# Kernel optimization log

Hardware: AMD Instinct MI355X
Metric: run time of the kernel (lower is better)

## Reference

```python
import jax, jax.numpy as jnp
import numpy as np

B, D, E, K, H, C = 8192, 1024, 8, 2, 2048, 512
LN_EPS = 1e-5


def setup_inputs() -> dict:
    key = jax.random.key(0)
    ks = jax.random.split(key, 6)
    s = 0.02
    return {
        "x": jax.random.normal(ks[0], (B, D), dtype=jnp.float32),
        "Wr": jax.random.normal(ks[1], (E, D), dtype=jnp.float32) * s,  # router weight [E,D]
        "br": jnp.zeros((E,), dtype=jnp.float32),
        "gamma": jnp.ones((E, D), dtype=jnp.float32),   # per-expert LayerNorm scale
        "beta": jnp.zeros((E, D), dtype=jnp.float32),   # per-expert LayerNorm shift
        "W1": jax.random.normal(ks[2], (E, H, D), dtype=jnp.float32) * s,
        "b1": jnp.zeros((E, H), dtype=jnp.float32),
        "W2": jax.random.normal(ks[3], (E, C, H), dtype=jnp.float32) * s,
        "b2": jnp.zeros((E, C), dtype=jnp.float32),
    }


def reference(x, Wr, br, gamma, beta, W1, b1, W2, b2):
    # Router + top-k gating (softmax over the k selected logits only)
    router_logits = x @ Wr.T + br                       # [B,E]
    topk_vals, topk_idx = jax.lax.top_k(router_logits, K)  # [B,K]
    topk_w = jax.nn.softmax(topk_vals, axis=-1)         # [B,K]
    # Dense gate [B,E]: gate[b,e] = sum_j topk_w[b,j] * (topk_idx[b,j]==e)
    gate = (jax.nn.one_hot(topk_idx, E, dtype=x.dtype) * topk_w[..., None]).sum(axis=1)

    # LayerNorm statistics are expert-independent; affine is per-expert
    mu = x.mean(axis=-1, keepdims=True)
    var = ((x - mu) ** 2).mean(axis=-1, keepdims=True)
    xn = (x - mu) * jax.lax.rsqrt(var + LN_EPS)          # [B,D]

    out = jnp.zeros((x.shape[0], C), dtype=x.dtype)
    for e in range(E):  # small fixed expert count
        xe = xn * gamma[e] + beta[e]                     # [B,D]
        h = jax.nn.gelu(xe @ W1[e].T + b1[e], approximate=False)  # [B,H]
        y = h @ W2[e].T + b2[e]                          # [B,C]
        out = out + gate[:, e:e + 1] * y
    return out
```

## Files before the change

kernel.cpp:

```cpp
#include <hip/hip_runtime.h>
#include <hip/hip_bf16.h>
#include <math.h>

#define B_TOK 8192
#define DDIM 1024
#define NEXP 8
#define HDIM 2048
#define CDIM 512
#define LN_EPS 1e-5f
#define MAXT256 72
#define MAXROWS (MAXT256 * 256)

typedef __attribute__((ext_vector_type(4))) float f32x4;
typedef __attribute__((ext_vector_type(8))) short bf16x8;

__device__ __forceinline__ unsigned short f2bf(float f) {
  __hip_bfloat16 h = __float2bfloat16(f);
  return *reinterpret_cast<unsigned short*>(&h);
}
__device__ __forceinline__ float bf2f(unsigned short u) {
  unsigned int x = ((unsigned int)u) << 16;
  return *reinterpret_cast<float*>(&x);
}

__device__ __forceinline__ float gelu_f(float v) {
  const float t = __builtin_fmaf(0.044715f * v, v, 1.0f);
  const float u = -1.5957691216f * v * t;
  return v * __builtin_amdgcn_rcpf(1.0f + __expf(u));
}

__device__ __forceinline__ void gload_lds16(const unsigned short* g, unsigned short* l) {
  __builtin_amdgcn_global_load_lds(
      (const __attribute__((address_space(1))) unsigned int*)g,
      (__attribute__((address_space(3))) unsigned int*)l, 16, 0, 0);
}

__global__ __launch_bounds__(256) void router_ln_kernel(
    const float* __restrict__ x, const float* __restrict__ Wr,
    const float* __restrict__ br, int* __restrict__ eidx,
    float* __restrict__ wgt, unsigned short* __restrict__ xn) {
  const int wid = threadIdx.x >> 6;
  const int lane = threadIdx.x & 63;
  const int tok = blockIdx.x * 4 + wid;

  const float4* xr = reinterpret_cast<const float4*>(x + (size_t)tok * DDIM);
  float4 xv[4];
  float sum = 0.f, sumsq = 0.f;
  float dot[NEXP];
#pragma unroll
  for (int e = 0; e < NEXP; ++e) dot[e] = 0.f;

#pragma unroll
  for (int i = 0; i < 4; ++i) {
    const int f = i * 64 + lane;
    float4 v = xr[f];
    xv[i] = v;
    sum += v.x + v.y + v.z + v.w;
    sumsq += v.x * v.x + v.y * v.y + v.z * v.z + v.w * v.w;
#pragma unroll
    for (int e = 0; e < NEXP; ++e) {
      float4 w = reinterpret_cast<const float4*>(Wr + e * DDIM)[f];
      dot[e] += v.x * w.x + v.y * w.y + v.z * w.z + v.w * w.w;
    }
  }
#pragma unroll
  for (int off = 32; off > 0; off >>= 1) {
    sum += __shfl_xor(sum, off);
    sumsq += __shfl_xor(sumsq, off);
#pragma unroll
    for (int e = 0; e < NEXP; ++e) dot[e] += __shfl_xor(dot[e], off);
  }
  const float mu = sum * (1.f / DDIM);
  const float var = sumsq * (1.f / DDIM) - mu * mu;
  const float rs = rsqrtf(var + LN_EPS);

  float lg[NEXP];
#pragma unroll
  for (int e = 0; e < NEXP; ++e) lg[e] = dot[e] + br[e];

  int i1 = 0; float v1 = lg[0];
#pragma unroll
  for (int e = 1; e < NEXP; ++e) { if (lg[e] > v1) { v1 = lg[e]; i1 = e; } }
  int i2 = -1; float v2 = -3.4e38f;
#pragma unroll
  for (int e = 0; e < NEXP; ++e) { if (e != i1 && lg[e] > v2) { v2 = lg[e]; i2 = e; } }

  const float e2 = __expf(v2 - v1);
  const float inv = 1.f / (1.f + e2);
  if (lane == 0) {
    eidx[tok * 2] = i1; eidx[tok * 2 + 1] = i2;
    wgt[tok * 2] = inv; wgt[tok * 2 + 1] = e2 * inv;
  }

  unsigned short* xnr = xn + (size_t)tok * DDIM;
#pragma unroll
  for (int i = 0; i < 4; ++i) {
    const int f = i * 64 + lane;
    float4 v = xv[i];
    ushort4 o;
    o.x = f2bf((v.x - mu) * rs);
    o.y = f2bf((v.y - mu) * rs);
    o.z = f2bf((v.z - mu) * rs);
    o.w = f2bf((v.w - mu) * rs);
    reinterpret_cast<ushort4*>(xnr)[f] = o;
  }
}

__global__ __launch_bounds__(256) void sort_kernel(
    const int* __restrict__ eidx,
    int* __restrict__ tokRow,
    int* __restrict__ slot2row,
    int* __restrict__ tileExp,
    int* __restrict__ nTilesOut) {
  __shared__ int cnt[NEXP], segBase[NEXP], cur[NEXP];
  const int tid = threadIdx.x;
  if (tid < NEXP) { cnt[tid] = 0; cur[tid] = 0; }
  __syncthreads();
  for (int t = tid; t < B_TOK * 2; t += 256)
    atomicAdd(&cnt[eidx[t]], 1);
  __syncthreads();
  if (tid == 0) {
    int c = 0;
    for (int e = 0; e < NEXP; ++e) {
      segBase[e] = c;
      const int nt = (cnt[e] + 255) >> 8;
      for (int t = 0; t < nt; ++t) tileExp[(c >> 8) + t] = e;
      for (int p = c + cnt[e]; p < c + nt * 256; ++p) tokRow[p] = 0;
      c += nt * 256;
    }
    *nTilesOut = c >> 8;
  }
  __syncthreads();
  for (int t = tid; t < B_TOK * 2; t += 256) {
    const int e = eidx[t];
    const int pos = segBase[e] + atomicAdd(&cur[e], 1);
    tokRow[pos] = t >> 1;
    slot2row[t] = pos;
  }
}

__global__ __launch_bounds__(256) void prep_w1_kernel(
    const float* __restrict__ W1, const float* __restrict__ gamma,
    const float* __restrict__ beta, const float* __restrict__ b1,
    unsigned short* __restrict__ W1g, float* __restrict__ c1) {
  const int eh = blockIdx.x;
  const int e = eh >> 11;
  const int tid = threadIdx.x;

  float4 w = reinterpret_cast<const float4*>(W1 + (size_t)eh * DDIM)[tid];
  float4 g = reinterpret_cast<const float4*>(gamma + (size_t)e * DDIM)[tid];
  float4 bt = reinterpret_cast<const float4*>(beta + (size_t)e * DDIM)[tid];

  ushort4 o;
  o.x = f2bf(w.x * g.x); o.y = f2bf(w.y * g.y);
  o.z = f2bf(w.z * g.z); o.w = f2bf(w.w * g.w);
  reinterpret_cast<ushort4*>(W1g + (size_t)eh * DDIM)[tid] = o;

  float p = w.x * bt.x + w.y * bt.y + w.z * bt.z + w.w * bt.w;
#pragma unroll
  for (int off = 32; off > 0; off >>= 1) p += __shfl_xor(p, off);
  __shared__ float red[4];
  const int lane = tid & 63, wv = tid >> 6;
  if (lane == 0) red[wv] = p;
  __syncthreads();
  if (tid == 0) c1[eh] = b1[eh] + red[0] + red[1] + red[2] + red[3];
}

__global__ __launch_bounds__(256) void prep_w2_kernel(
    const float* __restrict__ W2, unsigned short* __restrict__ W2b) {
  const int idx = blockIdx.x * 256 + threadIdx.x;
  float4 w = reinterpret_cast<const float4*>(W2)[idx];
  ushort4 o;
  o.x = f2bf(w.x); o.y = f2bf(w.y); o.z = f2bf(w.z); o.w = f2bf(w.w);
  reinterpret_cast<ushort4*>(W2b)[idx] = o;
}

#define BM 128
#define BN 128
#define BKK 64

__global__ __launch_bounds__(256) void gemm1_gelu_kernel(
    const unsigned short* __restrict__ A,
    const unsigned short* __restrict__ W1g,
    const float* __restrict__ c1,
    const int* __restrict__ tokRow, const int* __restrict__ tileExp,
    const int* __restrict__ nTiles,
    unsigned short* __restrict__ Hout) {
  const int flat = blockIdx.x;
  const int by = flat & 15;
  const int bx = flat >> 4;
  if ((bx >> 1) >= *nTiles) return;
  const int e = tileExp[bx >> 1];

  __shared__ unsigned short lA[BM * BKK];
  __shared__ unsigned short lB[BN * BKK];
  const int tid = threadIdx.x;
  const int lane = tid & 63;
  const int wid = tid >> 6;
  const int wr = wid >> 1, wc = wid & 1;
  const int l15 = lane & 15, l4 = lane >> 4;

  const unsigned short* Bbase = W1g + ((size_t)e * HDIM + (size_t)by * BN) * DDIM;

  const int r = tid >> 3;
  const int swz = ((tid & 7) ^ (r & 7)) * 8;
  const int dst = (tid & 7) * 8;
  int aRow[4];
#pragma unroll
  for (int i = 0; i < 4; ++i) aRow[i] = tokRow[bx * BM + i * 32 + r];

  f32x4 acc[4][4];
#pragma unroll
  for (int n = 0; n < 4; ++n)
#pragma unroll
    for (int m = 0; m < 4; ++m)
#pragma unroll
      for (int j = 0; j < 4; ++j) acc[n][m][j] = 0.f;

  for (int k0 = 0; k0 < DDIM; k0 += BKK) {
#pragma unroll
    for (int i = 0; i < 4; ++i)
      gload_lds16(A + (size_t)aRow[i] * DDIM + k0 + swz,
                  &lA[(i * 32 + r) * BKK + dst]);
#pragma unroll
    for (int i = 0; i < 4; ++i)
      gload_lds16(Bbase + (size_t)(i * 32 + r) * DDIM + k0 + swz,
                  &lB[(i * 32 + r) * BKK + dst]);
    __syncthreads();
#pragma unroll
    for (int kk = 0; kk < 2; ++kk) {
      bf16x8 xf[4], wf[4];
      const int slot = (((kk * 4 + l4) ^ (l15 & 7)) * 8);
#pragma unroll
      for (int m = 0; m < 4; ++m)
        xf[m] = *reinterpret_cast<const bf16x8*>(
            &lA[(wr * 64 + m * 16 + l15) * BKK + slot]);
#pragma unroll
      for (int n = 0; n < 4; ++n)
        wf[n] = *reinterpret_cast<const bf16x8*>(
            &lB[(wc * 64 + n * 16 + l15) * BKK + slot]);
#pragma unroll
      for (int n = 0; n < 4; ++n)
#pragma unroll
        for (int m = 0; m < 4; ++m)
          acc[n][m] = __builtin_amdgcn_mfma_f32_16x16x32_bf16(wf[n], xf[m], acc[n][m], 0, 0, 0);
    }
    __syncthreads();
  }

  const int row0 = bx * BM + wr * 64;
  const int col0 = by * BN + wc * 64;
  const float* biasp = c1 + e * HDIM;
#pragma unroll
  for (int n = 0; n < 4; ++n) {
    const int hb = col0 + n * 16 + l4 * 4;
    const float4 b4 = *reinterpret_cast<const float4*>(biasp + hb);
#pragma unroll
    for (int m = 0; m < 4; ++m) {
      const int tokr = row0 + m * 16 + l15;
      ushort4 o;
      o.x = f2bf(gelu_f(acc[n][m][0] + b4.x));
      o.y = f2bf(gelu_f(acc[n][m][1] + b4.y));
      o.z = f2bf(gelu_f(acc[n][m][2] + b4.z));
      o.w = f2bf(gelu_f(acc[n][m][3] + b4.w));
      *reinterpret_cast<ushort4*>(&Hout[(size_t)tokr * HDIM + hb]) = o;
    }
  }
}

#define BM2 128
#define BN2 64

__global__ __launch_bounds__(256) void gemm2_kernel(
    const unsigned short* __restrict__ Hbuf,
    const unsigned short* __restrict__ W2b,
    const int* __restrict__ tileExp, const int* __restrict__ nTiles,
    unsigned short* __restrict__ Y) {
  const int flat = blockIdx.x;
  const int by = flat & 7;
  const int bx = flat >> 3;
  if ((bx >> 1) >= *nTiles) return;
  const int e = tileExp[bx >> 1];

  __shared__ unsigned short lA[BM2 * BKK];
  __shared__ unsigned short lB[BN2 * BKK];
  const int tid = threadIdx.x;
  const int lane = tid & 63;
  const int wid = tid >> 6;
  const int wr = wid >> 1, wc = wid & 1;
  const int l15 = lane & 15, l4 = lane >> 4;

  const unsigned short* Abase = Hbuf + (size_t)bx * BM2 * HDIM;
  const unsigned short* Bbase = W2b + ((size_t)e * CDIM + (size_t)by * BN2) * HDIM;

  f32x4 acc[2][4];
#pragma unroll
  for (int n = 0; n < 2; ++n)
#pragma unroll
    for (int m = 0; m < 4; ++m)
#pragma unroll
      for (int j = 0; j < 4; ++j) acc[n][m][j] = 0.f;

  const int r = tid >> 3;
  const int swz = ((tid & 7) ^ (r & 7)) * 8;
  const int dst = (tid & 7) * 8;

  for (int k0 = 0; k0 < HDIM; k0 += BKK) {
#pragma unroll
    for (int i = 0; i < 4; ++i)
      gload_lds16(Abase + (size_t)(i * 32 + r) * HDIM + k0 + swz,
                  &lA[(i * 32 + r) * BKK + dst]);
#pragma unroll
    for (int i = 0; i < 2; ++i)
      gload_lds16(Bbase + (size_t)(i * 32 + r) * HDIM + k0 + swz,
                  &lB[(i * 32 + r) * BKK + dst]);
    __syncthreads();
#pragma unroll
    for (int kk = 0; kk < 2; ++kk) {
      bf16x8 xf[4], wf[2];
      const int slot = (((kk * 4 + l4) ^ (l15 & 7)) * 8);
#pragma unroll
      for (int m = 0; m < 4; ++m)
        xf[m] = *reinterpret_cast<const bf16x8*>(
            &lA[(wr * 64 + m * 16 + l15) * BKK + slot]);
#pragma unroll
      for (int n = 0; n < 2; ++n)
        wf[n] = *reinterpret_cast<const bf16x8*>(
            &lB[(wc * 32 + n * 16 + l15) * BKK + slot]);
#pragma unroll
      for (int n = 0; n < 2; ++n)
#pragma unroll
        for (int m = 0; m < 4; ++m)
          acc[n][m] = __builtin_amdgcn_mfma_f32_16x16x32_bf16(wf[n], xf[m], acc[n][m], 0, 0, 0);
    }
    __syncthreads();
  }

  const int row0 = bx * BM2 + wr * 64;
  const int col0 = by * BN2 + wc * 32;
#pragma unroll
  for (int n = 0; n < 2; ++n) {
    const int cb = col0 + n * 16 + l4 * 4;
#pragma unroll
    for (int m = 0; m < 4; ++m) {
      const int tokr = row0 + m * 16 + l15;
      ushort4 o;
      o.x = f2bf(acc[n][m][0]);
      o.y = f2bf(acc[n][m][1]);
      o.z = f2bf(acc[n][m][2]);
      o.w = f2bf(acc[n][m][3]);
      *reinterpret_cast<ushort4*>(&Y[(size_t)tokr * CDIM + cb]) = o;
    }
  }
}

__global__ __launch_bounds__(256) void combine_kernel(
    const unsigned short* __restrict__ Y, const int* __restrict__ slot2row,
    const int* __restrict__ eidx, const float* __restrict__ wgt,
    const float* __restrict__ b2, float* __restrict__ out) {
  const int idx = blockIdx.x * 256 + threadIdx.x;
  const int b = idx >> 7;
  const int c4 = (idx & 127) * 4;
  const int r0 = slot2row[b * 2], r1 = slot2row[b * 2 + 1];
  const int e0 = eidx[b * 2], e1 = eidx[b * 2 + 1];
  const float w0 = wgt[b * 2], w1 = wgt[b * 2 + 1];
  ushort4 y0 = *reinterpret_cast<const ushort4*>(Y + (size_t)r0 * CDIM + c4);
  ushort4 y1 = *reinterpret_cast<const ushort4*>(Y + (size_t)r1 * CDIM + c4);
  float4 bb0 = *reinterpret_cast<const float4*>(b2 + e0 * CDIM + c4);
  float4 bb1 = *reinterpret_cast<const float4*>(b2 + e1 * CDIM + c4);
  float4 o;
  o.x = w0 * (bf2f(y0.x) + bb0.x) + w1 * (bf2f(y1.x) + bb1.x);
  o.y = w0 * (bf2f(y0.y) + bb0.y) + w1 * (bf2f(y1.y) + bb1.y);
  o.z = w0 * (bf2f(y0.z) + bb0.z) + w1 * (bf2f(y1.z) + bb1.z);
  o.w = w0 * (bf2f(y0.w) + bb0.w) + w1 * (bf2f(y1.w) + bb1.w);
  *reinterpret_cast<float4*>(out + (size_t)b * CDIM + c4) = o;
}

extern "C" void kernel_launch(void* const* d_in, const int* in_sizes, int n_in,
                              void* d_out, int out_size, void* d_ws, size_t ws_size,
                              hipStream_t stream) {
  const float* x     = (const float*)d_in[0];
  const float* Wr    = (const float*)d_in[1];
  const float* br    = (const float*)d_in[2];
  const float* gamma = (const float*)d_in[3];
  const float* beta  = (const float*)d_in[4];
  const float* W1    = (const float*)d_in[5];
  const float* b1    = (const float*)d_in[6];
  const float* W2    = (const float*)d_in[7];
  const float* b2    = (const float*)d_in[8];
  float* out = (float*)d_out;

  char* ws = (char*)d_ws;
  unsigned short* xn   = (unsigned short*)(ws);
  unsigned short* W2b  = (unsigned short*)(ws);
  unsigned short* hbuf = (unsigned short*)(ws + (size_t)16 * 1048576);
  unsigned short* W1g  = (unsigned short*)(ws + (size_t)88 * 1048576);
  unsigned short* ybuf = (unsigned short*)(ws + (size_t)88 * 1048576);
  char* misc           = ws + (size_t)120 * 1048576;
  float* c1      = (float*)(misc);
  int* eidx      = (int*)(misc + 65536);
  float* wgt     = (float*)(misc + 2 * 65536);
  int* slot2row  = (int*)(misc + 3 * 65536);
  int* tokRow    = (int*)(misc + 4 * 65536);
  int* tileExp   = (int*)(misc + 4 * 65536 + 131072);
  int* nTiles    = tileExp + MAXT256;

  router_ln_kernel<<<dim3(B_TOK / 4), dim3(256), 0, stream>>>(x, Wr, br, eidx, wgt, xn);
  sort_kernel<<<dim3(1), dim3(256), 0, stream>>>(eidx, tokRow, slot2row, tileExp, nTiles);
  prep_w1_kernel<<<dim3(NEXP * HDIM), dim3(256), 0, stream>>>(W1, gamma, beta, b1, W1g, c1);

  gemm1_gelu_kernel<<<dim3(2304), dim3(256), 0, stream>>>(
      xn, W1g, c1, tokRow, tileExp, nTiles, hbuf);

  prep_w2_kernel<<<dim3((NEXP * CDIM * HDIM / 4) / 256), dim3(256), 0, stream>>>(W2, W2b);

  gemm2_kernel<<<dim3(1152), dim3(256), 0, stream>>>(
      hbuf, W2b, tileExp, nTiles, ybuf);
  combine_kernel<<<dim3(B_TOK * CDIM / 4 / 256), dim3(256), 0, stream>>>(
      ybuf, slot2row, eidx, wgt, b2, out);
}
```

Baseline: 303.7 us.

## Load gemm1 activations directly to registers and enlarge gemm2 tiles to 128x128

In gemm1, the gathered activation rows are no longer staged through LDS. Each lane now loads its MFMA fragments for the whole K-step straight from global memory into registers, while only the weight tile goes through LDS. Gemm2 moves from 128x64 to 128x128 tiles with a remapped block index, halving the grid so each block reuses its A tile across more output columns. The change trades LDS traffic and a barrier dependency for uncoalesced global loads in gemm1, and gives gemm2 more accumulator registers per thread and fewer blocks.

Result: slower. 335.7 us (+10.5%).

```diff
diff --git a/kernel.cpp b/kernel.cpp
--- a/kernel.cpp
+++ b/kernel.cpp
@@ -192,7 +192,6 @@
   if ((bx >> 1) >= *nTiles) return;
   const int e = tileExp[bx >> 1];
 
-  __shared__ unsigned short lA[BM * BKK];
   __shared__ unsigned short lB[BN * BKK];
   const int tid = threadIdx.x;
   const int lane = tid & 63;
@@ -205,9 +204,11 @@
   const int r = tid >> 3;
   const int swz = ((tid & 7) ^ (r & 7)) * 8;
   const int dst = (tid & 7) * 8;
-  int aRow[4];
-#pragma unroll
-  for (int i = 0; i < 4; ++i) aRow[i] = tokRow[bx * BM + i * 32 + r];
+
+  const unsigned short* aPtr[4];
+#pragma unroll
+  for (int m = 0; m < 4; ++m)
+    aPtr[m] = A + (size_t)tokRow[bx * BM + wr * 64 + m * 16 + l15] * DDIM + l4 * 8;
 
   f32x4 acc[4][4];
 #pragma unroll
@@ -218,23 +219,21 @@
       for (int j = 0; j < 4; ++j) acc[n][m][j] = 0.f;
 
   for (int k0 = 0; k0 < DDIM; k0 += BKK) {
-#pragma unroll
-    for (int i = 0; i < 4; ++i)
-      gload_lds16(A + (size_t)aRow[i] * DDIM + k0 + swz,
-                  &lA[(i * 32 + r) * BKK + dst]);
 #pragma unroll
     for (int i = 0; i < 4; ++i)
       gload_lds16(Bbase + (size_t)(i * 32 + r) * DDIM + k0 + swz,
                   &lB[(i * 32 + r) * BKK + dst]);
+    bf16x8 xf[4][2];
+#pragma unroll
+    for (int m = 0; m < 4; ++m)
+#pragma unroll
+      for (int kk = 0; kk < 2; ++kk)
+        xf[m][kk] = *reinterpret_cast<const bf16x8*>(aPtr[m] + k0 + kk * 32);
     __syncthreads();
 #pragma unroll
     for (int kk = 0; kk < 2; ++kk) {
-      bf16x8 xf[4], wf[4];
+      bf16x8 wf[4];
       const int slot = (((kk * 4 + l4) ^ (l15 & 7)) * 8);
-#pragma unroll
-      for (int m = 0; m < 4; ++m)
-        xf[m] = *reinterpret_cast<const bf16x8*>(
-            &lA[(wr * 64 + m * 16 + l15) * BKK + slot]);
 #pragma unroll
       for (int n = 0; n < 4; ++n)
         wf[n] = *reinterpret_cast<const bf16x8*>(
@@ -243,7 +242,7 @@
       for (int n = 0; n < 4; ++n)
 #pragma unroll
         for (int m = 0; m < 4; ++m)
-          acc[n][m] = __builtin_amdgcn_mfma_f32_16x16x32_bf16(wf[n], xf[m], acc[n][m], 0, 0, 0);
+          acc[n][m] = __builtin_amdgcn_mfma_f32_16x16x32_bf16(wf[n], xf[m][kk], acc[n][m], 0, 0, 0);
     }
     __syncthreads();
   }
@@ -268,34 +267,33 @@
   }
 }
 
-#define BM2 128
-#define BN2 64
-
 __global__ __launch_bounds__(256) void gemm2_kernel(
     const unsigned short* __restrict__ Hbuf,
     const unsigned short* __restrict__ W2b,
     const int* __restrict__ tileExp, const int* __restrict__ nTiles,
     unsigned short* __restrict__ Y) {
   const int flat = blockIdx.x;
-  const int by = flat & 7;
-  const int bx = flat >> 3;
+  const int p = flat & 7;
+  const int q = flat >> 3;
+  const int by = p >> 1;
+  const int bx = (p & 1) * 72 + q;
   if ((bx >> 1) >= *nTiles) return;
   const int e = tileExp[bx >> 1];
 
-  __shared__ unsigned short lA[BM2 * BKK];
-  __shared__ unsigned short lB[BN2 * BKK];
+  __shared__ unsigned short lA[BM * BKK];
+  __shared__ unsigned short lB[BN * BKK];
   const int tid = threadIdx.x;
   const int lane = tid & 63;
   const int wid = tid >> 6;
   const int wr = wid >> 1, wc = wid & 1;
   const int l15 = lane & 15, l4 = lane >> 4;
 
-  const unsigned short* Abase = Hbuf + (size_t)bx * BM2 * HDIM;
-  const unsigned short* Bbase = W2b + ((size_t)e * CDIM + (size_t)by * BN2) * HDIM;
-
-  f32x4 acc[2][4];
-#pragma unroll
-  for (int n = 0; n < 2; ++n)
+  const unsigned short* Abase = Hbuf + (size_t)bx * BM * HDIM;
+  const unsigned short* Bbase = W2b + ((size_t)e * CDIM + (size_t)by * BN) * HDIM;
+
+  f32x4 acc[4][4];
+#pragma unroll
+  for (int n = 0; n < 4; ++n)
 #pragma unroll
     for (int m = 0; m < 4; ++m)
 #pragma unroll
@@ -311,24 +309,24 @@
       gload_lds16(Abase + (size_t)(i * 32 + r) * HDIM + k0 + swz,
                   &lA[(i * 32 + r) * BKK + dst]);
 #pragma unroll
-    for (int i = 0; i < 2; ++i)
+    for (int i = 0; i < 4; ++i)
       gload_lds16(Bbase + (size_t)(i * 32 + r) * HDIM + k0 + swz,
                   &lB[(i * 32 + r) * BKK + dst]);
     __syncthreads();
 #pragma unroll
     for (int kk = 0; kk < 2; ++kk) {
-      bf16x8 xf[4], wf[2];
+      bf16x8 xf[4], wf[4];
       const int slot = (((kk * 4 + l4) ^ (l15 & 7)) * 8);
 #pragma unroll
       for (int m = 0; m < 4; ++m)
         xf[m] = *reinterpret_cast<const bf16x8*>(
             &lA[(wr * 64 + m * 16 + l15) * BKK + slot]);
 #pragma unroll
-      for (int n = 0; n < 2; ++n)
+      for (int n = 0; n < 4; ++n)
         wf[n] = *reinterpret_cast<const bf16x8*>(
-            &lB[(wc * 32 + n * 16 + l15) * BKK + slot]);
-#pragma unroll
-      for (int n = 0; n < 2; ++n)
+            &lB[(wc * 64 + n * 16 + l15) * BKK + slot]);
+#pragma unroll
+      for (int n = 0; n < 4; ++n)
 #pragma unroll
         for (int m = 0; m < 4; ++m)
           acc[n][m] = __builtin_amdgcn_mfma_f32_16x16x32_bf16(wf[n], xf[m], acc[n][m], 0, 0, 0);
@@ -336,10 +334,10 @@
     __syncthreads();
   }
 
-  const int row0 = bx * BM2 + wr * 64;
-  const int col0 = by * BN2 + wc * 32;
-#pragma unroll
-  for (int n = 0; n < 2; ++n) {
+  const int row0 = bx * BM + wr * 64;
+  const int col0 = by * BN + wc * 64;
+#pragma unroll
+  for (int n = 0; n < 4; ++n) {
     const int cb = col0 + n * 16 + l4 * 4;
 #pragma unroll
     for (int m = 0; m < 4; ++m) {
@@ -414,7 +412,7 @@
 
   prep_w2_kernel<<<dim3((NEXP * CDIM * HDIM / 4) / 256), dim3(256), 0, stream>>>(W2, W2b);
 
-  gemm2_kernel<<<dim3(1152), dim3(256), 0, stream>>>(
+  gemm2_kernel<<<dim3(576), dim3(256), 0, stream>>>(
       hbuf, W2b, tileExp, nTiles, ybuf);
   combine_kernel<<<dim3(B_TOK * CDIM / 4 / 256), dim3(256), 0, stream>>>(
       ybuf, slot2row, eidx, wgt, b2, out);
```
